# Kernel optimization log

Hardware: AMD Instinct MI355X
Metric: run time of the kernel (lower is better)

## Reference

```python
import jax, jax.numpy as jnp
import numpy as np

N = 8192        # num nodes, > sparse_attention_threshold=5000 -> sparse attention path
IN = 128        # in_channels
OUT = 128       # out_channels
HEADS = 2       # attention_heads
DEG = 32        # avg degree used to build theta sparsity


def _xavier(key, shape):
    a = np.sqrt(6.0 / (shape[0] + shape[1])).astype(np.float32)
    return jax.random.uniform(key, shape, jnp.float32, -a, a)


def setup_inputs() -> dict:
    rng = np.random.default_rng(0)
    rows = np.repeat(np.arange(N), DEG)
    cols = rng.integers(0, N, size=N * DEG)
    theta_np = np.zeros((N, N), dtype=np.float32)
    theta_np[rows, cols] = 1.0
    # matches torch: rows, cols = np.where(theta > 1e-5)
    r, c = np.nonzero(theta_np > 1e-5)
    edge_index = jnp.asarray(np.stack([r, c]).astype(np.int32))  # [2, E]
    key = jax.random.key(0)
    ks = jax.random.split(key, 4)
    x = jax.random.normal(ks[0], (N, IN), jnp.float32)
    weight = _xavier(ks[1], (IN, OUT * HEADS))
    bias = jnp.zeros((OUT * HEADS,), jnp.float32)
    att_weight1 = _xavier(ks[2], (2 * OUT, OUT // 2))
    att_weight2 = _xavier(ks[3], (OUT // 2, 1))
    return {"x": x, "theta": jnp.asarray(theta_np), "weight": weight,
            "bias": bias, "att_weight1": att_weight1,
            "att_weight2": att_weight2, "edge_index": edge_index}


def _forward(x, weight, bias, att_weight1, att_weight2, edge_index):
    # x @ W + b, reshape to [N, heads, out]
    h = (x @ weight + bias).reshape(N, HEADS, OUT)
    src, dst = edge_index[0], edge_index[1]
    # cat([h_src, h_dst]) @ W1 == h_src @ W1[:OUT] + h_dst @ W1[OUT:]
    # project at node level first (cheaper), then gather per edge
    p_src = jnp.einsum('nhd,df->nhf', h, att_weight1[:OUT])
    p_dst = jnp.einsum('nhd,df->nhf', h, att_weight1[OUT:])
    s = jax.nn.leaky_relu(p_src[src] + p_dst[dst])               # [E, H, OUT//2]
    scores = jnp.einsum('ehf,fo->eho', s, att_weight2)[..., 0]    # [E, H]
    # torch does F.softmax(att_scores, dim=0): GLOBAL softmax over all edges per head
    att = jax.nn.softmax(scores, axis=0)                          # [E, H]
    # sparse COO mm: out[src] += att * h[dst]
    msgs = att[:, :, None] * h[dst]                               # [E, H, OUT]
    agg = jnp.zeros((N, HEADS, OUT), h.dtype).at[src].add(msgs)
    return agg.mean(axis=1)                                       # mean over heads -> [N, OUT]


def reference(x, theta, weight, bias, att_weight1, att_weight2, edge_index):
    # theta only determines the edge list (computed on CPU/numpy in the torch
    # code); edge_index is precomputed consistently in setup_inputs.
    del theta
    return _forward(x, weight, bias, att_weight1, att_weight2, edge_index)
```

## Files before the change

### kernel.cpp

```cpp
#include <hip/hip_runtime.h>
#include <hip/hip_bf16.h>

#define NN 8192
#define INC 128
#define HC 256
#define NPB 16
#define NGRP (NN / NPB)
#define APB 4
#define AGRID (NN / APB)
#define SCALE_BLOCKS 512
#define MAXDEG 32

__global__ __launch_bounds__(256) void k_h_p(
    const float* __restrict__ x, const float* __restrict__ W,
    const float* __restrict__ bias, const float* __restrict__ att1,
    const int* __restrict__ ei, float* __restrict__ h,
    float* __restrict__ ps, float* __restrict__ pd,
    int* __restrict__ offs, int E) {
  int t = threadIdx.x;
  int n0 = blockIdx.x * NPB;
  for (int e = blockIdx.x * 256 + t; e < E; e += NGRP * 256) {
    if (e == 0) offs[0] = 0;
    else { int s1 = ei[e]; if (s1 != ei[e - 1]) offs[s1] = e; }
    if (e == E - 1) offs[NN] = E;
  }
  __shared__ float xs[NPB * INC];
  __shared__ float hs[NPB * HC];
  {
    const float4* xin = (const float4*)(x + (size_t)n0 * INC);
    ((float4*)xs)[t] = xin[t];
    ((float4*)xs)[t + 256] = xin[t + 256];
  }
  __syncthreads();
  int cg = t & 63, ng = t >> 6;
  {
    float4 b4 = *(const float4*)&bias[cg * 4];
    float4 a0 = b4, a1 = b4, a2 = b4, a3 = b4;
    const float* xr0 = xs + (ng * 4 + 0) * INC;
    const float* xr1 = xs + (ng * 4 + 1) * INC;
    const float* xr2 = xs + (ng * 4 + 2) * INC;
    const float* xr3 = xs + (ng * 4 + 3) * INC;
    #pragma unroll 4
    for (int d = 0; d < INC; ++d) {
      float4 w4 = *(const float4*)&W[d * HC + cg * 4];
      float x0 = xr0[d], x1 = xr1[d], x2 = xr2[d], x3 = xr3[d];
      a0.x += x0 * w4.x; a0.y += x0 * w4.y; a0.z += x0 * w4.z; a0.w += x0 * w4.w;
      a1.x += x1 * w4.x; a1.y += x1 * w4.y; a1.z += x1 * w4.z; a1.w += x1 * w4.w;
      a2.x += x2 * w4.x; a2.y += x2 * w4.y; a2.z += x2 * w4.z; a2.w += x2 * w4.w;
      a3.x += x3 * w4.x; a3.y += x3 * w4.y; a3.z += x3 * w4.z; a3.w += x3 * w4.w;
    }
    float4* hb = (float4*)&hs[(ng * 4) * HC + cg * 4];
    *(float4*)&h[(size_t)(n0 + ng * 4 + 0) * HC + cg * 4] = a0;
    *(float4*)&h[(size_t)(n0 + ng * 4 + 1) * HC + cg * 4] = a1;
    *(float4*)&h[(size_t)(n0 + ng * 4 + 2) * HC + cg * 4] = a2;
    *(float4*)&h[(size_t)(n0 + ng * 4 + 3) * HC + cg * 4] = a3;
    hb[0] = a0; hb[HC / 4] = a1; hb[2 * HC / 4] = a2; hb[3 * HC / 4] = a3;
  }
  __syncthreads();
  {
    int fg = cg & 15, sel = cg >> 4;
    int head = sel & 1, isdst = sel >> 1;
    const float* a1p = att1 + isdst * 128 * 64 + fg * 4;
    float4 p0 = {0,0,0,0}, p1 = {0,0,0,0}, p2 = {0,0,0,0}, p3 = {0,0,0,0};
    const float* hr0 = hs + (ng * 4 + 0) * HC + head * 128;
    const float* hr1 = hs + (ng * 4 + 1) * HC + head * 128;
    const float* hr2 = hs + (ng * 4 + 2) * HC + head * 128;
    const float* hr3 = hs + (ng * 4 + 3) * HC + head * 128;
    #pragma unroll 4
    for (int d = 0; d < 128; ++d) {
      float4 a4 = *(const float4*)&a1p[d * 64];
      float h0 = hr0[d], h1 = hr1[d], h2 = hr2[d], h3 = hr3[d];
      p0.x += h0 * a4.x; p0.y += h0 * a4.y; p0.z += h0 * a4.z; p0.w += h0 * a4.w;
      p1.x += h1 * a4.x; p1.y += h1 * a4.y; p1.z += h1 * a4.z; p1.w += h1 * a4.w;
      p2.x += h2 * a4.x; p2.y += h2 * a4.y; p2.z += h2 * a4.z; p2.w += h2 * a4.w;
      p3.x += h3 * a4.x; p3.y += h3 * a4.y; p3.z += h3 * a4.z; p3.w += h3 * a4.w;
    }
    float* dp = isdst ? pd : ps;
    *(float4*)&dp[(size_t)(n0 + ng * 4 + 0) * 128 + head * 64 + fg * 4] = p0;
    *(float4*)&dp[(size_t)(n0 + ng * 4 + 1) * 128 + head * 64 + fg * 4] = p1;
    *(float4*)&dp[(size_t)(n0 + ng * 4 + 2) * 128 + head * 64 + fg * 4] = p2;
    *(float4*)&dp[(size_t)(n0 + ng * 4 + 3) * 128 + head * 64 + fg * 4] = p3;
  }
}

__global__ __launch_bounds__(256) void k_agg(
    const float* __restrict__ h, const float* __restrict__ ps,
    const float* __restrict__ pd, const int* __restrict__ ei,
    const float* __restrict__ att2, const int* __restrict__ offs,
    float* __restrict__ raw, float* __restrict__ part, int E) {
  int t = threadIdx.x, wid = t >> 6, lane = t & 63;
  int n = blockIdx.x * APB + wid;
  __shared__ float w2l[64];
  __shared__ int   dstl[APB][MAXDEG];
  __shared__ float evl[APB][2][MAXDEG];
  if (t < 64) w2l[t] = att2[t];
  int lo = offs[n], hi = offs[n + 1];
  int m = hi - lo;
  if (lane < m) dstl[wid][lane] = ei[E + lo + lane];
  __syncthreads();
  int head = lane >> 5, j = lane & 31;
  float2 psv = *(const float2*)&ps[(size_t)n * 128 + head * 64 + j * 2];
  float wa = w2l[j * 2], wb = w2l[j * 2 + 1];
  float rsum = 0.f;
  #pragma unroll 4
  for (int i = 0; i < m; ++i) {
    int dst = dstl[wid][i];
    float2 pdv = *(const float2*)&pd[(size_t)dst * 128 + head * 64 + j * 2];
    float v0 = psv.x + pdv.x; v0 = v0 > 0.f ? v0 : 0.01f * v0;
    float v1 = psv.y + pdv.y; v1 = v1 > 0.f ? v1 : 0.01f * v1;
    float sc = v0 * wa + v1 * wb;
    sc += __shfl_xor(sc, 1);  sc += __shfl_xor(sc, 2);  sc += __shfl_xor(sc, 4);
    sc += __shfl_xor(sc, 8);  sc += __shfl_xor(sc, 16);
    float ev = __expf(sc);
    if (j == 0) { evl[wid][head][i] = ev; rsum += ev; }
  }
  if (j == 0) part[n * 2 + head] = rsum;
  __syncthreads();
  const float* evh = evl[wid][head];
  float4 a0 = {0,0,0,0}, a1 = {0,0,0,0};
  int i = 0;
  for (; i + 2 <= m; i += 2) {
    float e0 = evh[i], e1 = evh[i + 1];
    float4 h0 = *(const float4*)&h[(size_t)dstl[wid][i] * HC + lane * 4];
    float4 h1 = *(const float4*)&h[(size_t)dstl[wid][i + 1] * HC + lane * 4];
    a0.x += e0 * h0.x; a0.y += e0 * h0.y; a0.z += e0 * h0.z; a0.w += e0 * h0.w;
    a1.x += e1 * h1.x; a1.y += e1 * h1.y; a1.z += e1 * h1.z; a1.w += e1 * h1.w;
  }
  if (i < m) {
    float e0 = evh[i];
    float4 h0 = *(const float4*)&h[(size_t)dstl[wid][i] * HC + lane * 4];
    a0.x += e0 * h0.x; a0.y += e0 * h0.y; a0.z += e0 * h0.z; a0.w += e0 * h0.w;
  }
  float4 res;
  res.x = a0.x + a1.x; res.y = a0.y + a1.y;
  res.z = a0.z + a1.z; res.w = a0.w + a1.w;
  *(float4*)&raw[(size_t)n * HC + lane * 4] = res;
}

__global__ __launch_bounds__(256) void k_scale(
    const float* __restrict__ raw, const float* __restrict__ part,
    float* __restrict__ out) {
  int t = threadIdx.x;
  float s0 = 0.f, s1 = 0.f;
  #pragma unroll 4
  for (int k = 0; k < 32; ++k) {
    float2 p = ((const float2*)part)[t + 256 * k];
    s0 += p.x; s1 += p.y;
  }
  #pragma unroll
  for (int off = 1; off <= 32; off <<= 1) {
    s0 += __shfl_xor(s0, off);
    s1 += __shfl_xor(s1, off);
  }
  __shared__ float ws0[4], ws1[4];
  if ((t & 63) == 0) { ws0[t >> 6] = s0; ws1[t >> 6] = s1; }
  __syncthreads();
  float inv0 = 1.f / (ws0[0] + ws0[1] + ws0[2] + ws0[3]);
  float inv1 = 1.f / (ws1[0] + ws1[1] + ws1[2] + ws1[3]);
  const float4* r4 = (const float4*)raw;
  float4* o4 = (float4*)out;
  int idx = blockIdx.x * 256 + t;
  #pragma unroll
  for (int rep = 0; rep < 2; ++rep, idx += SCALE_BLOCKS * 256) {
    int nn = idx >> 5, c4 = idx & 31;
    float4 a = r4[nn * 64 + c4];
    float4 b = r4[nn * 64 + 32 + c4];
    float4 o;
    o.x = 0.5f * (a.x * inv0 + b.x * inv1);
    o.y = 0.5f * (a.y * inv0 + b.y * inv1);
    o.z = 0.5f * (a.z * inv0 + b.z * inv1);
    o.w = 0.5f * (a.w * inv0 + b.w * inv1);
    o4[idx] = o;
  }
}

extern "C" void kernel_launch(void* const* d_in, const int* in_sizes, int n_in,
                              void* d_out, int out_size, void* d_ws, size_t ws_size,
                              hipStream_t stream) {
  const float* x    = (const float*)d_in[0];
  const float* W    = (const float*)d_in[2];
  const float* bias = (const float*)d_in[3];
  const float* att1 = (const float*)d_in[4];
  const float* att2 = (const float*)d_in[5];
  const int* ei = (const int*)d_in[6];
  int E = in_sizes[6] / 2;
  float* out = (float*)d_out;

  float* ws = (float*)d_ws;
  float* h    = ws;
  float* ps   = h  + (size_t)NN * HC;
  float* pd   = ps + (size_t)NN * 128;
  float* raw  = pd + (size_t)NN * 128;
  float* part = raw + (size_t)NN * HC;
  int*   offs = (int*)(part + (size_t)NN * 2);

  k_h_p<<<NGRP, 256, 0, stream>>>(x, W, bias, att1, ei, h, ps, pd, offs, E);
  k_agg<<<AGRID, 256, 0, stream>>>(h, ps, pd, ei, att2, offs, raw, part, E);
  k_scale<<<SCALE_BLOCKS, 256, 0, stream>>>(raw, part, out);
}
```

Baseline: 378.6 us.

## Fuse edge score and aggregation loops in k_agg, vectorize LDS reads in k_h_p

The aggregation kernel now computes each edge's attention score and exp inside the same loop that gathers h rows. This removes the shared-memory staging of exp values, the second pass and the extra __syncthreads, and lets the pd and h gathers for two edges be issued together. The projection GEMMs in k_h_p now read x/h from LDS as float4 with an inner unrolled loop, which cuts LDS instruction count. The fused loop raises register pressure per iteration, and the softmax partial sum is now written after the gather loop.

```diff
diff --git a/kernel.cpp b/kernel.cpp
--- a/kernel.cpp
+++ b/kernel.cpp
@@ -40,14 +40,25 @@
     const float* xr1 = xs + (ng * 4 + 1) * INC;
     const float* xr2 = xs + (ng * 4 + 2) * INC;
     const float* xr3 = xs + (ng * 4 + 3) * INC;
-    #pragma unroll 4
-    for (int d = 0; d < INC; ++d) {
-      float4 w4 = *(const float4*)&W[d * HC + cg * 4];
-      float x0 = xr0[d], x1 = xr1[d], x2 = xr2[d], x3 = xr3[d];
-      a0.x += x0 * w4.x; a0.y += x0 * w4.y; a0.z += x0 * w4.z; a0.w += x0 * w4.w;
-      a1.x += x1 * w4.x; a1.y += x1 * w4.y; a1.z += x1 * w4.z; a1.w += x1 * w4.w;
-      a2.x += x2 * w4.x; a2.y += x2 * w4.y; a2.z += x2 * w4.z; a2.w += x2 * w4.w;
-      a3.x += x3 * w4.x; a3.y += x3 * w4.y; a3.z += x3 * w4.z; a3.w += x3 * w4.w;
+    #pragma unroll 2
+    for (int d = 0; d < INC; d += 4) {
+      float4 xv0 = *(const float4*)&xr0[d];
+      float4 xv1 = *(const float4*)&xr1[d];
+      float4 xv2 = *(const float4*)&xr2[d];
+      float4 xv3 = *(const float4*)&xr3[d];
+      const float* f0 = (const float*)&xv0;
+      const float* f1 = (const float*)&xv1;
+      const float* f2 = (const float*)&xv2;
+      const float* f3 = (const float*)&xv3;
+      #pragma unroll
+      for (int k = 0; k < 4; ++k) {
+        float4 w4 = *(const float4*)&W[(size_t)(d + k) * HC + cg * 4];
+        float x0 = f0[k], x1 = f1[k], x2 = f2[k], x3 = f3[k];
+        a0.x += x0 * w4.x; a0.y += x0 * w4.y; a0.z += x0 * w4.z; a0.w += x0 * w4.w;
+        a1.x += x1 * w4.x; a1.y += x1 * w4.y; a1.z += x1 * w4.z; a1.w += x1 * w4.w;
+        a2.x += x2 * w4.x; a2.y += x2 * w4.y; a2.z += x2 * w4.z; a2.w += x2 * w4.w;
+        a3.x += x3 * w4.x; a3.y += x3 * w4.y; a3.z += x3 * w4.z; a3.w += x3 * w4.w;
+      }
     }
     float4* hb = (float4*)&hs[(ng * 4) * HC + cg * 4];
     *(float4*)&h[(size_t)(n0 + ng * 4 + 0) * HC + cg * 4] = a0;
@@ -66,14 +77,25 @@
     const float* hr1 = hs + (ng * 4 + 1) * HC + head * 128;
     const float* hr2 = hs + (ng * 4 + 2) * HC + head * 128;
     const float* hr3 = hs + (ng * 4 + 3) * HC + head * 128;
-    #pragma unroll 4
-    for (int d = 0; d < 128; ++d) {
-      float4 a4 = *(const float4*)&a1p[d * 64];
-      float h0 = hr0[d], h1 = hr1[d], h2 = hr2[d], h3 = hr3[d];
-      p0.x += h0 * a4.x; p0.y += h0 * a4.y; p0.z += h0 * a4.z; p0.w += h0 * a4.w;
-      p1.x += h1 * a4.x; p1.y += h1 * a4.y; p1.z += h1 * a4.z; p1.w += h1 * a4.w;
-      p2.x += h2 * a4.x; p2.y += h2 * a4.y; p2.z += h2 * a4.z; p2.w += h2 * a4.w;
-      p3.x += h3 * a4.x; p3.y += h3 * a4.y; p3.z += h3 * a4.z; p3.w += h3 * a4.w;
+    #pragma unroll 2
+    for (int d = 0; d < 128; d += 4) {
+      float4 hv0 = *(const float4*)&hr0[d];
+      float4 hv1 = *(const float4*)&hr1[d];
+      float4 hv2 = *(const float4*)&hr2[d];
+      float4 hv3 = *(const float4*)&hr3[d];
+      const float* g0 = (const float*)&hv0;
+      const float* g1 = (const float*)&hv1;
+      const float* g2 = (const float*)&hv2;
+      const float* g3 = (const float*)&hv3;
+      #pragma unroll
+      for (int k = 0; k < 4; ++k) {
+        float4 a4 = *(const float4*)&a1p[(size_t)(d + k) * 64];
+        float h0 = g0[k], h1 = g1[k], h2 = g2[k], h3 = g3[k];
+        p0.x += h0 * a4.x; p0.y += h0 * a4.y; p0.z += h0 * a4.z; p0.w += h0 * a4.w;
+        p1.x += h1 * a4.x; p1.y += h1 * a4.y; p1.z += h1 * a4.z; p1.w += h1 * a4.w;
+        p2.x += h2 * a4.x; p2.y += h2 * a4.y; p2.z += h2 * a4.z; p2.w += h2 * a4.w;
+        p3.x += h3 * a4.x; p3.y += h3 * a4.y; p3.z += h3 * a4.z; p3.w += h3 * a4.w;
+      }
     }
     float* dp = isdst ? pd : ps;
     *(float4*)&dp[(size_t)(n0 + ng * 4 + 0) * 128 + head * 64 + fg * 4] = p0;
@@ -92,7 +114,6 @@
   int n = blockIdx.x * APB + wid;
   __shared__ float w2l[64];
   __shared__ int   dstl[APB][MAXDEG];
-  __shared__ float evl[APB][2][MAXDEG];
   if (t < 64) w2l[t] = att2[t];
   int lo = offs[n], hi = offs[n + 1];
   int m = hi - lo;
@@ -102,35 +123,44 @@
   float2 psv = *(const float2*)&ps[(size_t)n * 128 + head * 64 + j * 2];
   float wa = w2l[j * 2], wb = w2l[j * 2 + 1];
   float rsum = 0.f;
-  #pragma unroll 4
-  for (int i = 0; i < m; ++i) {
-    int dst = dstl[wid][i];
-    float2 pdv = *(const float2*)&pd[(size_t)dst * 128 + head * 64 + j * 2];
-    float v0 = psv.x + pdv.x; v0 = v0 > 0.f ? v0 : 0.01f * v0;
-    float v1 = psv.y + pdv.y; v1 = v1 > 0.f ? v1 : 0.01f * v1;
-    float sc = v0 * wa + v1 * wb;
-    sc += __shfl_xor(sc, 1);  sc += __shfl_xor(sc, 2);  sc += __shfl_xor(sc, 4);
-    sc += __shfl_xor(sc, 8);  sc += __shfl_xor(sc, 16);
-    float ev = __expf(sc);
-    if (j == 0) { evl[wid][head][i] = ev; rsum += ev; }
-  }
-  if (j == 0) part[n * 2 + head] = rsum;
-  __syncthreads();
-  const float* evh = evl[wid][head];
-  float4 a0 = {0,0,0,0}, a1 = {0,0,0,0};
+  float4 a0 = {0, 0, 0, 0}, a1 = {0, 0, 0, 0};
   int i = 0;
+  #pragma unroll 2
   for (; i + 2 <= m; i += 2) {
-    float e0 = evh[i], e1 = evh[i + 1];
-    float4 h0 = *(const float4*)&h[(size_t)dstl[wid][i] * HC + lane * 4];
-    float4 h1 = *(const float4*)&h[(size_t)dstl[wid][i + 1] * HC + lane * 4];
+    int d0 = dstl[wid][i], d1 = dstl[wid][i + 1];
+    float2 q0 = *(const float2*)&pd[(size_t)d0 * 128 + head * 64 + j * 2];
+    float2 q1 = *(const float2*)&pd[(size_t)d1 * 128 + head * 64 + j * 2];
+    float4 h0 = *(const float4*)&h[(size_t)d0 * HC + lane * 4];
+    float4 h1 = *(const float4*)&h[(size_t)d1 * HC + lane * 4];
+    float u0 = psv.x + q0.x; u0 = u0 > 0.f ? u0 : 0.01f * u0;
+    float u1 = psv.y + q0.y; u1 = u1 > 0.f ? u1 : 0.01f * u1;
+    float s0 = u0 * wa + u1 * wb;
+    float v0 = psv.x + q1.x; v0 = v0 > 0.f ? v0 : 0.01f * v0;
+    float v1 = psv.y + q1.y; v1 = v1 > 0.f ? v1 : 0.01f * v1;
+    float s1 = v0 * wa + v1 * wb;
+    s0 += __shfl_xor(s0, 1);  s0 += __shfl_xor(s0, 2);  s0 += __shfl_xor(s0, 4);
+    s0 += __shfl_xor(s0, 8);  s0 += __shfl_xor(s0, 16);
+    s1 += __shfl_xor(s1, 1);  s1 += __shfl_xor(s1, 2);  s1 += __shfl_xor(s1, 4);
+    s1 += __shfl_xor(s1, 8);  s1 += __shfl_xor(s1, 16);
+    float e0 = __expf(s0), e1 = __expf(s1);
+    rsum += e0; rsum += e1;
     a0.x += e0 * h0.x; a0.y += e0 * h0.y; a0.z += e0 * h0.z; a0.w += e0 * h0.w;
     a1.x += e1 * h1.x; a1.y += e1 * h1.y; a1.z += e1 * h1.z; a1.w += e1 * h1.w;
   }
   if (i < m) {
-    float e0 = evh[i];
-    float4 h0 = *(const float4*)&h[(size_t)dstl[wid][i] * HC + lane * 4];
+    int d0 = dstl[wid][i];
+    float2 q0 = *(const float2*)&pd[(size_t)d0 * 128 + head * 64 + j * 2];
+    float4 h0 = *(const float4*)&h[(size_t)d0 * HC + lane * 4];
+    float u0 = psv.x + q0.x; u0 = u0 > 0.f ? u0 : 0.01f * u0;
+    float u1 = psv.y + q0.y; u1 = u1 > 0.f ? u1 : 0.01f * u1;
+    float s0 = u0 * wa + u1 * wb;
+    s0 += __shfl_xor(s0, 1);  s0 += __shfl_xor(s0, 2);  s0 += __shfl_xor(s0, 4);
+    s0 += __shfl_xor(s0, 8);  s0 += __shfl_xor(s0, 16);
+    float e0 = __expf(s0);
+    rsum += e0;
     a0.x += e0 * h0.x; a0.y += e0 * h0.y; a0.z += e0 * h0.z; a0.w += e0 * h0.w;
   }
+  if (j == 0) part[n * 2 + head] = rsum;
   float4 res;
   res.x = a0.x + a1.x; res.y = a0.y + a1.y;
   res.z = a0.z + a1.z; res.w = a0.w + a1.w;
```

After: 364.6 us. -3.7%, faster.
